# Performance work log

Hardware: AMD Instinct MI355X
Metric: run time of the kernel (lower is better)

The kernel has to match this reference:

```python
import jax, jax.numpy as jnp
import numpy as np

WS = 7      # window size
SHIFT = 3   # shift size
NH = 6      # num heads
C = 192     # channels
HH = 56
WW = 56
B = 32


def _rel_coords():
    ch, cw = np.meshgrid(np.arange(WS), np.arange(WS), indexing='ij')
    coords = np.stack([ch, cw]).reshape(2, -1)            # (2, 49)
    rel = coords[:, :, None] - coords[:, None, :]          # (2, 49, 49)
    rel[0] += WS - 1
    rel[1] += WS - 1
    rel[0] *= 2 * WS - 1
    return rel.sum(0)                                      # (49, 49)


def _swin_attn_mask(Hp, Wp):
    img = np.zeros((Hp, Wp), np.int32)
    cnt = 0
    for hs in (slice(0, -WS), slice(-WS, -SHIFT), slice(-SHIFT, None)):
        for ws_ in (slice(0, -WS), slice(-WS, -SHIFT), slice(-SHIFT, None)):
            img[hs, ws_] = cnt
            cnt += 1
    win = img.reshape(Hp // WS, WS, Wp // WS, WS).transpose(0, 2, 1, 3).reshape(-1, WS * WS)
    return win[:, :, None] != win[:, None, :]              # (Nw, 49, 49) bool


def setup_inputs() -> dict:
    key = jax.random.key(0)
    ks = jax.random.split(key, 8)
    s = 0.02
    return {
        'x': jax.random.normal(ks[0], (B, HH * WW, C), jnp.float32),
        'H': HH,
        'W': WW,
        'attn_mask': jnp.asarray(_swin_attn_mask(HH, WW)),
        'relative_coords': jnp.asarray(_rel_coords(), jnp.int32),
        'norm1_w': jnp.ones((C,), jnp.float32),
        'norm1_b': jnp.zeros((C,), jnp.float32),
        'qkv_w': jax.random.normal(ks[1], (3 * C, C), jnp.float32) * s,
        'rel_bias': jax.random.normal(ks[2], ((2 * WS - 1) ** 2, NH), jnp.float32) * 0.2,
        'proj_w': jax.random.normal(ks[3], (C, C), jnp.float32) * s,
        'proj_b': jnp.zeros((C,), jnp.float32),
        'norm2_w': jnp.ones((C,), jnp.float32),
        'norm2_b': jnp.zeros((C,), jnp.float32),
        'fc1_w': jax.random.normal(ks[4], (4 * C, C), jnp.float32) * s,
        'fc1_b': jnp.zeros((4 * C,), jnp.float32),
        'fc2_w': jax.random.normal(ks[5], (C, 4 * C), jnp.float32) * s,
        'fc2_b': jnp.zeros((C,), jnp.float32),
    }


def _ln(t, w, b):
    m = t.mean(-1, keepdims=True)
    v = t.var(-1, keepdims=True)
    return (t - m) / jnp.sqrt(v + 1e-5) * w + b


def reference(x, H, W, attn_mask, relative_coords, norm1_w, norm1_b, qkv_w, rel_bias,
              proj_w, proj_b, norm2_w, norm2_b, fc1_w, fc1_b, fc2_w, fc2_b):
    Bb, L, Cd = x.shape
    nh, hd = NH, C // NH
    shortcut = x
    h = _ln(x, norm1_w, norm1_b).reshape(Bb, H, W, Cd)
    pad_h = (WS - H % WS) % WS
    pad_w = (WS - W % WS) % WS
    if pad_h or pad_w:
        h = jnp.pad(h, ((0, 0), (0, pad_h), (0, pad_w), (0, 0)))
    Hp, Wp = H + pad_h, W + pad_w
    if SHIFT > 0:
        h = jnp.roll(h, (-SHIFT, -SHIFT), axis=(1, 2))
    nWh, nWw = Hp // WS, Wp // WS
    Lw = WS * WS
    win = h.reshape(Bb, nWh, WS, nWw, WS, Cd).transpose(0, 1, 3, 2, 4, 5).reshape(-1, Lw, Cd)
    B_ = win.shape[0]
    qkv = (win @ qkv_w.T).reshape(B_, Lw, 3, nh, hd).transpose(2, 0, 3, 1, 4)
    q, k, v = qkv[0], qkv[1], qkv[2]
    # NOTE: source multiplies by num_dim**0.5 (faithful quirk)
    attn = jnp.einsum('bhid,bhjd->bhij', q, k) * (Cd ** 0.5)
    bias = rel_bias[relative_coords].transpose(2, 0, 1)    # (nh, Lw, Lw)
    attn = attn + bias[None]
    if SHIFT > 0:
        Nw = attn_mask.shape[0]
        attn = attn.reshape(-1, Nw, nh, Lw, Lw)
        attn = jnp.where(attn_mask[None, :, None], -100.0, attn)
        attn = attn.reshape(B_, nh, Lw, Lw)
    attn = jax.nn.softmax(attn, axis=-1)
    out = jnp.einsum('bhij,bhjd->bhid', attn, v).transpose(0, 2, 1, 3).reshape(B_, Lw, Cd)
    out = out @ proj_w.T + proj_b
    out = out.reshape(Bb, nWh, nWw, WS, WS, Cd).transpose(0, 1, 3, 2, 4, 5).reshape(Bb, Hp, Wp, Cd)
    if SHIFT > 0:
        out = jnp.roll(out, (SHIFT, SHIFT), axis=(1, 2))
    out = out[:, :H, :W].reshape(Bb, L, Cd)
    x = shortcut + out
    h2 = _ln(x, norm2_w, norm2_b)
    h2 = jax.nn.gelu(h2 @ fc1_w.T + fc1_b, approximate=False)
    # source MLP applies GELU (drop2 = act_layer()) after fc2 (faithful quirk)
    h2 = jax.nn.gelu(h2 @ fc2_w.T + fc2_b, approximate=False)
    return x + h2
```

## Files before the change

### kernel.cpp

```cpp
#include <hip/hip_runtime.h>

#define WS7    7
#define SHIFT3 3
#define NHEAD  6
#define CCH    192
#define HDIM   32
#define HH56   56
#define LTOK   (HH56*HH56)
#define NWIN   64
#define NBATCH 32
#define NWTOT  (NBATCH*NWIN)
#define LW     49
#define MTOK   (NWTOT*LW)

typedef unsigned short u16;
typedef unsigned int   u32;
typedef __bf16 b16;
typedef b16   b16x8 __attribute__((ext_vector_type(8)));
typedef u16   u16x8 __attribute__((ext_vector_type(8)));
typedef float f32x4 __attribute__((ext_vector_type(4)));

__device__ __forceinline__ float b2f(u16 u) {
    u32 x = ((u32)u) << 16;
    return __builtin_bit_cast(float, x);
}
__device__ __forceinline__ u16 f2b(float f) {
    u32 x = __builtin_bit_cast(u32, f);
    u32 r = x + 0x7FFFu + ((x >> 16) & 1u);
    return (u16)(r >> 16);
}
__device__ __forceinline__ float gelu_exact(float x) {
    return 0.5f * x * (1.0f + erff(x * 0.7071067811865475f));
}

__device__ __forceinline__ int map_token(int m, int &b) {
    int widx = m / LW, p = m - widx * LW;
    b = widx >> 6;
    int wloc = widx & 63;
    int wh = wloc >> 3, ww = wloc & 7;
    int i = p / WS7, j = p - i * WS7;
    int gh = wh * WS7 + i + SHIFT3; if (gh >= HH56) gh -= HH56;
    int gw = ww * WS7 + j + SHIFT3; if (gw >= HH56) gw -= HH56;
    return gh * HH56 + gw;
}

__global__ __launch_bounds__(1024) void probe_kernel(const u16* __restrict__ x, int* flag) {
    __shared__ int ch, cz;
    if (threadIdx.x == 0) { ch = 0; cz = 0; }
    __syncthreads();
    int i = threadIdx.x * 16;
    u16x8 a = *(const u16x8*)(x + i);
    u16x8 b = *(const u16x8*)(x + i + 8);
    int h = 0, z = 0;
    #pragma unroll
    for (int q = 0; q < 8; q++) {
        h += (((a[q] >> 7) & 0xFF) >= 0xC0) + (((b[q] >> 7) & 0xFF) >= 0xC0);
        z += (a[q] == 0) + (b[q] == 0);
    }
    #pragma unroll
    for (int off = 32; off > 0; off >>= 1) {
        h += __shfl_xor(h, off, 64);
        z += __shfl_xor(z, off, 64);
    }
    if ((threadIdx.x & 63) == 0) { atomicAdd(&ch, h); atomicAdd(&cz, z); }
    __syncthreads();
    if (threadIdx.x == 0) *flag = (ch > 250 || cz > 2048) ? 1 : 0;
}

#define CANON_TOTAL 445302
__global__ __launch_bounds__(256) void canon_all_kernel(
    const int* __restrict__ flag,
    const void* s0, const void* s1, const void* s2,  const void* s3,
    const void* s4, const void* s5, const void* s6,  const void* s7,
    const void* s8, const void* s9, const void* s10, const void* s11,
    char* __restrict__ ws)
{
    int i = blockIdx.x * 256 + threadIdx.x;
    if (i >= CANON_TOTAL) return;
    const void* srcs[12] = {s0, s1, s2, s3, s4, s5, s6, s7, s8, s9, s10, s11};
    const int cnt[12] = {110592, 36864, 147456, 147456, 192, 192, 192, 192, 192, 768, 192, 1014};
    const int off[12] = {64, 221248, 294976, 589888, 884800, 885184, 885568, 885952, 886336, 886720, 888256, 888640};
    int seg = 0, base = 0;
    while (seg < 11 && i >= base + cnt[seg]) { base += cnt[seg]; seg++; }
    int j = i - base;
    const void* sp = srcs[seg];
    u16* dp = (u16*)(ws + off[seg]);
    dp[j] = (*flag) ? f2b(((const float*)sp)[j]) : ((const u16*)sp)[j];
}

__device__ __forceinline__ void stage192(const u16* __restrict__ g, int ldg, u16* s, int tid) {
    #pragma unroll
    for (int it = 0; it < 7; it++) {
        int t = it * 256 + tid;
        if (t < 1600) {
            int row = t / 25, c = t - row * 25;
            int cc = (c == 24) ? 0 : c;
            const u16* src = g + (size_t)row * ldg + cc * 8;
            u16* dst = s + (size_t)(it * 256 + (tid & ~63)) * 8;
            __builtin_amdgcn_global_load_lds(
                (const __attribute__((address_space(1))) void*)src,
                (__attribute__((address_space(3))) void*)dst, 16, 0, 0);
        }
    }
}

__device__ __forceinline__ void ln_lds_rows(u16* As, const u16* __restrict__ w,
                                            const u16* __restrict__ bia, int tid) {
    int r = tid >> 2, p = tid & 3;
    u16* row = As + r * 200 + p * 48;
    u16x8 vv[6];
    float s = 0.f, sq = 0.f;
    #pragma unroll
    for (int j = 0; j < 6; j++) {
        vv[j] = *(const u16x8*)(row + j * 8);
        #pragma unroll
        for (int q = 0; q < 8; q++) { float f = b2f(vv[j][q]); s += f; sq += f * f; }
    }
    s  += __shfl_xor(s, 1, 64);  s  += __shfl_xor(s, 2, 64);
    sq += __shfl_xor(sq, 1, 64); sq += __shfl_xor(sq, 2, 64);
    float mean = s * (1.f / 192.f);
    float var  = fmaxf(sq * (1.f / 192.f) - mean * mean, 0.f);
    float rstd = rsqrtf(var + 1e-5f);
    #pragma unroll
    for (int j = 0; j < 6; j++) {
        u16x8 o;
        #pragma unroll
        for (int q = 0; q < 8; q++) {
            int col = p * 48 + j * 8 + q;
            o[q] = f2b((b2f(vv[j][q]) - mean) * rstd * b2f(w[col]) + b2f(bia[col]));
        }
        *(u16x8*)(row + j * 8) = o;
    }
}

__device__ __forceinline__ void gather_ln(const void* __restrict__ xsrc, int isf,
                                          int mtile, const u16* __restrict__ w,
                                          const u16* __restrict__ bia,
                                          u16* As, int tid) {
    int r = tid >> 2, p = tid & 3;
    int b; int l = map_token(mtile + r, b);
    size_t rowoff = ((size_t)b * LTOK + l) * CCH + p * 48;
    float v[48];
    if (isf) {
        const float* xp = (const float*)xsrc + rowoff;
        #pragma unroll
        for (int j = 0; j < 12; j++) {
            float4 f = *(const float4*)(xp + j * 4);
            v[j * 4 + 0] = f.x; v[j * 4 + 1] = f.y;
            v[j * 4 + 2] = f.z; v[j * 4 + 3] = f.w;
        }
    } else {
        const u16* xp = (const u16*)xsrc + rowoff;
        #pragma unroll
        for (int j = 0; j < 6; j++) {
            u16x8 u = *(const u16x8*)(xp + j * 8);
            #pragma unroll
            for (int q = 0; q < 8; q++) v[j * 8 + q] = b2f(u[q]);
        }
    }
    float s = 0.f, sq = 0.f;
    #pragma unroll
    for (int j = 0; j < 48; j++) { s += v[j]; sq += v[j] * v[j]; }
    s  += __shfl_xor(s, 1, 64);  s  += __shfl_xor(s, 2, 64);
    sq += __shfl_xor(sq, 1, 64); sq += __shfl_xor(sq, 2, 64);
    float mean = s * (1.f / 192.f);
    float var  = fmaxf(sq * (1.f / 192.f) - mean * mean, 0.f);
    float rstd = rsqrtf(var + 1e-5f);
    u16* row = As + r * 200 + p * 48;
    #pragma unroll
    for (int j = 0; j < 6; j++) {
        u16x8 o;
        #pragma unroll
        for (int q = 0; q < 8; q++) {
            int col = p * 48 + j * 8 + q;
            o[q] = f2b((v[j * 8 + q] - mean) * rstd * b2f(w[col]) + b2f(bia[col]));
        }
        *(u16x8*)(row + j * 8) = o;
    }
}

template<int MODE, int NT, int LNF>
__global__ __launch_bounds__(256) void gemm_k192(
    const u16* __restrict__ A, const u16* __restrict__ Bm, int N,
    const u16* __restrict__ lnw, const u16* __restrict__ lnb,
    const u16* __restrict__ bias,
    u16* __restrict__ Cb, u16* __restrict__ X1, const void* __restrict__ Xin,
    int m_base, const int* __restrict__ flag)
{
    __shared__ __align__(16) u16 As[64 * 200];
    __shared__ __align__(16) u16 Bs[2][64 * 200];
    int isf = *flag;
    int tid = threadIdx.x;
    int m0 = blockIdx.x * 64;
    int wave = tid >> 6, lane = tid & 63;
    int wm = wave >> 1, wn = wave & 1;
    int quad = lane >> 4, mr = lane & 15;

    stage192(Bm, 192, Bs[0], tid);
    if (MODE == 0) gather_ln(Xin, isf, m_base + m0, lnw, lnb, As, tid);
    else           stage192(A + (size_t)m0 * 192, 192, As, tid);
    __syncthreads();
    if (LNF) { ln_lds_rows(As, lnw, lnb, tid); __syncthreads(); }

    const u16* pa0 = &As[(wm * 32 + mr) * 200 + quad * 8];
    #pragma unroll 1
    for (int nb = 0; nb < NT; nb++) {
        if (nb + 1 < NT)
            stage192(Bm + (size_t)(nb + 1) * 64 * 192, 192, Bs[(nb + 1) & 1], tid);
        const u16* pb0 = &Bs[nb & 1][(wn * 32 + mr) * 200 + quad * 8];
        f32x4 acc00 = {}, acc01 = {}, acc10 = {}, acc11 = {};
        #pragma unroll
        for (int ks = 0; ks < 6; ks++) {
            b16x8 a0 = __builtin_bit_cast(b16x8, *(const u16x8*)(pa0 + ks * 32));
            b16x8 a1 = __builtin_bit_cast(b16x8, *(const u16x8*)(pa0 + 16 * 200 + ks * 32));
            b16x8 b0 = __builtin_bit_cast(b16x8, *(const u16x8*)(pb0 + ks * 32));
            b16x8 b1 = __builtin_bit_cast(b16x8, *(const u16x8*)(pb0 + 16 * 200 + ks * 32));
            acc00 = __builtin_amdgcn_mfma_f32_16x16x32_bf16(a0, b0, acc00, 0, 0, 0);
            acc01 = __builtin_amdgcn_mfma_f32_16x16x32_bf16(a0, b1, acc01, 0, 0, 0);
            acc10 = __builtin_amdgcn_mfma_f32_16x16x32_bf16(a1, b0, acc10, 0, 0, 0);
            acc11 = __builtin_amdgcn_mfma_f32_16x16x32_bf16(a1, b1, acc11, 0, 0, 0);
        }
        int n0 = nb * 64;
        f32x4 accs[2][2] = {{acc00, acc01}, {acc10, acc11}};
        #pragma unroll
        for (int sm = 0; sm < 2; sm++) {
            #pragma unroll
            for (int sn = 0; sn < 2; sn++) {
                f32x4 v = accs[sm][sn];
                int nn = n0 + wn * 32 + sn * 16 + mr;
                int mb = m0 + wm * 32 + sm * 16 + quad * 4;
                #pragma unroll
                for (int r = 0; r < 4; r++) {
                    int mm = mb + r;
                    float val = v[r];
                    if (MODE == 0) {
                        Cb[(size_t)mm * N + nn] = f2b(val);
                    } else if (MODE == 1) {
                        val += b2f(bias[nn]);
                        int b; int l = map_token(m_base + mm, b);
                        size_t idx = ((size_t)b * LTOK + l) * CCH + nn;
                        float xi = isf ? ((const float*)Xin)[idx] : b2f(((const u16*)Xin)[idx]);
                        X1[idx] = f2b(xi + val);
                    } else {
                        val = gelu_exact(val + b2f(bias[nn]));
                        Cb[(size_t)mm * N + nn] = f2b(val);
                    }
                }
            }
        }
        __syncthreads();
    }
}

__global__ __launch_bounds__(256) void gemm_k768(
    const u16* __restrict__ A, const u16* __restrict__ Bm,
    const u16* __restrict__ bias, const u16* __restrict__ X1,
    void* __restrict__ Oout, size_t o_off, const int* __restrict__ flag)
{
    __shared__ __align__(16) u16 As[64 * 200];
    __shared__ __align__(16) u16 Bs[2][64 * 200];
    int isf = *flag;
    int tid = threadIdx.x;
    int m0 = blockIdx.x * 64;
    int wave = tid >> 6, lane = tid & 63;
    int wm = wave >> 1, wn = wave & 1;
    int quad = lane >> 4, mr = lane & 15;

    f32x4 acc[3][4] = {};

    const u16* pa0 = &As[(wm * 32 + mr) * 200 + quad * 8];
    #pragma unroll 1
    for (int k0 = 0; k0 < 768; k0 += 192) {
        stage192(A + (size_t)m0 * 768 + k0, 768, As, tid);
        stage192(Bm + k0, 768, Bs[0], tid);
        __syncthreads();
        #pragma unroll
        for (int nb = 0; nb < 3; nb++) {
            if (nb < 2)
                stage192(Bm + (size_t)(nb + 1) * 64 * 768 + k0, 768, Bs[(nb + 1) & 1], tid);
            const u16* pb0 = &Bs[nb & 1][(wn * 32 + mr) * 200 + quad * 8];
            #pragma unroll
            for (int ks = 0; ks < 6; ks++) {
                b16x8 a0 = __builtin_bit_cast(b16x8, *(const u16x8*)(pa0 + ks * 32));
                b16x8 a1 = __builtin_bit_cast(b16x8, *(const u16x8*)(pa0 + 16 * 200 + ks * 32));
                b16x8 b0 = __builtin_bit_cast(b16x8, *(const u16x8*)(pb0 + ks * 32));
                b16x8 b1 = __builtin_bit_cast(b16x8, *(const u16x8*)(pb0 + 16 * 200 + ks * 32));
                acc[nb][0] = __builtin_amdgcn_mfma_f32_16x16x32_bf16(a0, b0, acc[nb][0], 0, 0, 0);
                acc[nb][1] = __builtin_amdgcn_mfma_f32_16x16x32_bf16(a0, b1, acc[nb][1], 0, 0, 0);
                acc[nb][2] = __builtin_amdgcn_mfma_f32_16x16x32_bf16(a1, b0, acc[nb][2], 0, 0, 0);
                acc[nb][3] = __builtin_amdgcn_mfma_f32_16x16x32_bf16(a1, b1, acc[nb][3], 0, 0, 0);
            }
            __syncthreads();
        }
    }

    #pragma unroll
    for (int nb = 0; nb < 3; nb++) {
        #pragma unroll
        for (int sm = 0; sm < 2; sm++) {
            #pragma unroll
            for (int sn = 0; sn < 2; sn++) {
                f32x4 v = acc[nb][sm * 2 + sn];
                int nn = nb * 64 + wn * 32 + sn * 16 + mr;
                int mb = m0 + wm * 32 + sm * 16 + quad * 4;
                #pragma unroll
                for (int r = 0; r < 4; r++) {
                    int mm = mb + r;
                    float val = gelu_exact(v[r] + b2f(bias[nn]));
                    size_t idx = (size_t)mm * CCH + nn;
                    float r2 = val + b2f(X1[idx]);
                    if (isf) ((float*)Oout)[o_off + idx] = r2;
                    else     ((u16*)Oout)[o_off + idx]  = f2b(r2);
                }
            }
        }
    }
}

__global__ __launch_bounds__(256) void attn_kernel(
    const u16* __restrict__ qkv, const u16* __restrict__ rel_bias,
    u16* __restrict__ aout)
{
    __shared__ __align__(16) u16 qs[64 * 32];
    __shared__ __align__(16) u16 ks[64 * 32];
    __shared__ __align__(16) u16 vsT[32 * 72];
    __shared__ __align__(16) u16 ps[64 * 72];
    __shared__ float bias_s[169];
    int blk = blockIdx.x;
    int widx = blk / NHEAD, head = blk - widx * NHEAD;
    int wloc = widx & 63;
    int wh = wloc >> 3, ww = wloc & 7;
    int tid = threadIdx.x;
    const u16* base = qkv + (size_t)widx * LW * 576 + head * HDIM;

    if (tid < 196) {
        int i = tid >> 2, c8 = (tid & 3) * 8;
        *(uint4*)&qs[i * 32 + c8] = *(const uint4*)(base + (size_t)i * 576 + c8);
        *(uint4*)&ks[i * 32 + c8] = *(const uint4*)(base + (size_t)i * 576 + 192 + c8);
        u16x8 vv = *(const u16x8*)(base + (size_t)i * 576 + 384 + c8);
        #pragma unroll
        for (int q = 0; q < 8; q++) vsT[(c8 + q) * 72 + i] = vv[q];
    }
    for (int idx = tid; idx < 32 * 15; idx += 256) {
        int d = idx / 15, j = 49 + (idx - d * 15);
        vsT[d * 72 + j] = 0;
    }
    if (tid < 169) bias_s[tid] = b2f(rel_bias[tid * NHEAD + head]);
    __syncthreads();

    int wave = tid >> 6, lane = tid & 63;
    int quad = lane >> 4, c = lane & 15;

    b16x8 aq = __builtin_bit_cast(b16x8, *(const u16x8*)&qs[(wave * 16 + c) * 32 + quad * 8]);
    f32x4 sacc[4];
    #pragma unroll
    for (int nt = 0; nt < 4; nt++) {
        b16x8 bk = __builtin_bit_cast(b16x8, *(const u16x8*)&ks[(nt * 16 + c) * 32 + quad * 8]);
        f32x4 z = {};
        sacc[nt] = __builtin_amdgcn_mfma_f32_16x16x32_bf16(aq, bk, z, 0, 0, 0);
    }

    const float SCALE = 13.856406460551018f;
    float val[4][4];
    int rbase = wave * 16 + quad * 4;
    #pragma unroll
    for (int r = 0; r < 4; r++) {
        int i = rbase + r;
        int ih = i / WS7, iw = i - ih * WS7;
        int ri = (wh == 7 ? (ih < 4 ? 1 : 2) : 0) * 3 + (ww == 7 ? (iw < 4 ? 1 : 2) : 0);
        #pragma unroll
        for (int nt = 0; nt < 4; nt++) {
            int j = nt * 16 + c;
            float v;
            if (i >= LW) v = 0.f;
            else if (j >= LW) v = -1e30f;
            else {
                int jh = j / WS7, jw = j - jh * WS7;
                int rj = (wh == 7 ? (jh < 4 ? 1 : 2) : 0) * 3 + (ww == 7 ? (jw < 4 ? 1 : 2) : 0);
                if (ri != rj) v = -100.0f;
                else v = fmaf(sacc[nt][r], SCALE, bias_s[(ih - jh + 6) * 13 + (iw - jw + 6)]);
            }
            val[r][nt] = v;
        }
    }

    #pragma unroll
    for (int r = 0; r < 4; r++) {
        float mx = fmaxf(fmaxf(val[r][0], val[r][1]), fmaxf(val[r][2], val[r][3]));
        for (int d = 1; d < 16; d <<= 1) mx = fmaxf(mx, __shfl_xor(mx, d, 64));
        float sum = 0.f;
        #pragma unroll
        for (int nt = 0; nt < 4; nt++) { float e = expf(val[r][nt] - mx); val[r][nt] = e; sum += e; }
        for (int d = 1; d < 16; d <<= 1) sum += __shfl_xor(sum, d, 64);
        float inv = 1.f / sum;
        int i = rbase + r;
        #pragma unroll
        for (int nt = 0; nt < 4; nt++)
            ps[i * 72 + nt * 16 + c] = f2b(val[r][nt] * inv);
    }

    f32x4 oacc[2] = {{}, {}};
    #pragma unroll
    for (int kh = 0; kh < 2; kh++) {
        b16x8 ap = __builtin_bit_cast(b16x8, *(const u16x8*)&ps[(wave * 16 + c) * 72 + kh * 32 + quad * 8]);
        #pragma unroll
        for (int nt = 0; nt < 2; nt++) {
            b16x8 bv = __builtin_bit_cast(b16x8, *(const u16x8*)&vsT[(nt * 16 + c) * 72 + kh * 32 + quad * 8]);
            oacc[nt] = __builtin_amdgcn_mfma_f32_16x16x32_bf16(ap, bv, oacc[nt], 0, 0, 0);
        }
    }
    #pragma unroll
    for (int nt = 0; nt < 2; nt++) {
        #pragma unroll
        for (int r = 0; r < 4; r++) {
            int i = rbase + r;
            if (i < LW)
                aout[((size_t)widx * LW + i) * CCH + head * HDIM + nt * 16 + c] = f2b(oacc[nt][r]);
        }
    }
}

extern "C" void kernel_launch(void* const* d_in, const int* in_sizes, int n_in,
                              void* d_out, int out_size, void* d_ws, size_t ws_size,
                              hipStream_t stream)
{
    const void* x_in = d_in[0];
    char* ws = (char*)d_ws;
    int* flag = (int*)ws;

    u16* qkvw_c  = (u16*)(ws + 64);
    u16* projw_c = (u16*)(ws + 221248);
    u16* fc1w_c  = (u16*)(ws + 294976);
    u16* fc2w_c  = (u16*)(ws + 589888);
    u16* n1w_c   = (u16*)(ws + 884800);
    u16* n1b_c   = (u16*)(ws + 885184);
    u16* n2w_c   = (u16*)(ws + 885568);
    u16* n2b_c   = (u16*)(ws + 885952);
    u16* projb_c = (u16*)(ws + 886336);
    u16* fc1b_c  = (u16*)(ws + 886720);
    u16* fc2b_c  = (u16*)(ws + 888256);
    u16* relb_c  = (u16*)(ws + 888640);

    const size_t P0 = 1u << 20;
    const size_t X1SZ   = (size_t)MTOK * CCH * 2;
    const size_t QKVSZ  = (size_t)MTOK * 576 * 2;
    const size_t H1FULL = (size_t)MTOK * 768 * 2;

    u16* x1 = (u16*)(ws + P0);

    probe_kernel<<<1, 1024, 0, stream>>>((const u16*)x_in, flag);
    canon_all_kernel<<<(CANON_TOTAL + 255) / 256, 256, 0, stream>>>(
        flag,
        d_in[7], d_in[9], d_in[13], d_in[15],
        d_in[5], d_in[6], d_in[11], d_in[12],
        d_in[10], d_in[14], d_in[16], d_in[8],
        ws);

    int QC, EC;
    u16 *aoutb, *qkvq, *h1q;
    if (ws_size >= P0 + 2 * X1SZ + H1FULL) {
        QC = 1; EC = 1;
        aoutb = (u16*)(ws + P0 + X1SZ);
        qkvq  = (u16*)(ws + P0 + 2 * X1SZ);
        h1q   = qkvq;
    } else if (ws_size >= P0 + 2 * X1SZ + QKVSZ) {
        QC = 1; EC = 2;
        aoutb = (u16*)(ws + P0 + X1SZ);
        qkvq  = (u16*)(ws + P0 + 2 * X1SZ);
        h1q   = qkvq;
    } else {
        QC = 4; EC = 8;
        aoutb = (u16*)(ws + P0 + X1SZ);
        qkvq  = (u16*)(ws + P0 + X1SZ + 9633792);
        h1q   = (u16*)(ws + P0 + X1SZ);
    }

    const int MQ = MTOK / QC;
    const int ME = MTOK / EC;

    for (int q = 0; q < QC; q++) {
        int mb = q * MQ;
        gemm_k192<0, 9, 0><<<MQ / 64, 256, 0, stream>>>(
            nullptr, qkvw_c, 576, n1w_c, n1b_c, nullptr, qkvq, nullptr, x_in, mb, flag);
        attn_kernel<<<(NWTOT / QC) * NHEAD, 256, 0, stream>>>(qkvq, relb_c, aoutb);
        gemm_k192<1, 3, 0><<<MQ / 64, 256, 0, stream>>>(
            aoutb, projw_c, 192, nullptr, nullptr, projb_c, nullptr, x1, x_in, mb, flag);
    }

    for (int e = 0; e < EC; e++) {
        size_t off = (size_t)e * ME * CCH;
        gemm_k192<2, 12, 1><<<ME / 64, 256, 0, stream>>>(
            x1 + off, fc1w_c, 768, n2w_c, n2b_c, fc1b_c, h1q, nullptr, nullptr, 0, flag);
        gemm_k768<<<ME / 64, 256, 0, stream>>>(
            h1q, fc2w_c, fc2b_c, x1 + off, d_out, off, flag);
    }
}
```

Measured before the change: 581.2 us.

## Rewrite fc2 GEMM with 128x192 tiles and async LDS double buffering

Replaces the fc2 GEMM (K=768) with a new templated kernel that uses 128x192 output tiles, a K-step of 32 and double-buffered shared memory. Tiles are filled with direct global-to-LDS loads using an XOR swizzle to avoid bank conflicts. The aim is more MFMA work per LDS read and overlap of the next tile's loads with the current step's math, replacing the old kernel that re-staged B three times per 192-wide K chunk. The trade-offs are higher register pressure from 24 accumulators per thread and half as many blocks, and correctness depends on the hand-written vmcnt waits.

```diff
diff --git a/kernel.cpp b/kernel.cpp
--- a/kernel.cpp
+++ b/kernel.cpp
@@ -252,66 +252,95 @@
     }
 }
 
-__global__ __launch_bounds__(256) void gemm_k768(
+template<int ROWS>
+__device__ __forceinline__ void stageL(const u16* __restrict__ g, int ldk, u16* s, int tid) {
+    constexpr int ITER = ROWS * 4 / 256;
+    #pragma unroll
+    for (int it = 0; it < ITER; it++) {
+        int t = it * 256 + tid;
+        int row = t >> 2, c = t & 3;
+        int cc = c ^ ((row >> 1) & 3);
+        const u16* src = g + (size_t)row * ldk + cc * 8;
+        u16* dst = s + (size_t)(it * 256 + (tid & ~63)) * 8;
+        __builtin_amdgcn_global_load_lds(
+            (const __attribute__((address_space(1))) void*)src,
+            (__attribute__((address_space(3))) void*)dst, 16, 0, 0);
+    }
+}
+
+template<int KK>
+__global__ __launch_bounds__(256, 3) void gemm_t3(
     const u16* __restrict__ A, const u16* __restrict__ Bm,
-    const u16* __restrict__ bias, const u16* __restrict__ X1,
-    void* __restrict__ Oout, size_t o_off, const int* __restrict__ flag)
+    const u16* __restrict__ bias,
+    const u16* __restrict__ X1,
+    void* __restrict__ Oout, size_t o_off,
+    const int* __restrict__ flag)
 {
-    __shared__ __align__(16) u16 As[64 * 200];
-    __shared__ __align__(16) u16 Bs[2][64 * 200];
-    int isf = *flag;
+    __shared__ __align__(16) u16 As[2][128 * 32];
+    __shared__ __align__(16) u16 Bs[2][192 * 32];
     int tid = threadIdx.x;
-    int m0 = blockIdx.x * 64;
+    int m0 = blockIdx.x * 128, n0 = blockIdx.y * 192;
     int wave = tid >> 6, lane = tid & 63;
     int wm = wave >> 1, wn = wave & 1;
     int quad = lane >> 4, mr = lane & 15;
 
-    f32x4 acc[3][4] = {};
-
-    const u16* pa0 = &As[(wm * 32 + mr) * 200 + quad * 8];
+    const u16* Ag = A + (size_t)m0 * KK;
+    const u16* Bg = Bm + (size_t)n0 * KK;
+
+    stageL<128>(Ag, KK, As[0], tid);
+    stageL<192>(Bg, KK, Bs[0], tid);
+
+    f32x4 acc[4][6] = {};
+    constexpr int NSTEP = KK / 32;
+
     #pragma unroll 1
-    for (int k0 = 0; k0 < 768; k0 += 192) {
-        stage192(A + (size_t)m0 * 768 + k0, 768, As, tid);
-        stage192(Bm + k0, 768, Bs[0], tid);
-        __syncthreads();
-        #pragma unroll
-        for (int nb = 0; nb < 3; nb++) {
-            if (nb < 2)
-                stage192(Bm + (size_t)(nb + 1) * 64 * 768 + k0, 768, Bs[(nb + 1) & 1], tid);
-            const u16* pb0 = &Bs[nb & 1][(wn * 32 + mr) * 200 + quad * 8];
+    for (int t = 0; t < NSTEP; t++) {
+        int cur = t & 1;
+        if (t + 1 < NSTEP) {
+            stageL<128>(Ag + (t + 1) * 32, KK, As[cur ^ 1], tid);
+            stageL<192>(Bg + (t + 1) * 32, KK, Bs[cur ^ 1], tid);
+            asm volatile("s_waitcnt vmcnt(5)");
+        } else {
+            asm volatile("s_waitcnt vmcnt(0)");
+        }
+        __builtin_amdgcn_s_barrier();
+        __builtin_amdgcn_sched_barrier(0);
+        b16x8 a[4], b[6];
+        #pragma unroll
+        for (int sm = 0; sm < 4; sm++) {
+            int row = wm * 64 + sm * 16 + mr;
+            a[sm] = __builtin_bit_cast(b16x8,
+                *(const u16x8*)&As[cur][row * 32 + (quad ^ ((row >> 1) & 3)) * 8]);
+        }
+        #pragma unroll
+        for (int sn = 0; sn < 6; sn++) {
+            int row = wn * 96 + sn * 16 + mr;
+            b[sn] = __builtin_bit_cast(b16x8,
+                *(const u16x8*)&Bs[cur][row * 32 + (quad ^ ((row >> 1) & 3)) * 8]);
+        }
+        #pragma unroll
+        for (int sm = 0; sm < 4; sm++)
             #pragma unroll
-            for (int ks = 0; ks < 6; ks++) {
-                b16x8 a0 = __builtin_bit_cast(b16x8, *(const u16x8*)(pa0 + ks * 32));
-                b16x8 a1 = __builtin_bit_cast(b16x8, *(const u16x8*)(pa0 + 16 * 200 + ks * 32));
-                b16x8 b0 = __builtin_bit_cast(b16x8, *(const u16x8*)(pb0 + ks * 32));
-                b16x8 b1 = __builtin_bit_cast(b16x8, *(const u16x8*)(pb0 + 16 * 200 + ks * 32));
-                acc[nb][0] = __builtin_amdgcn_mfma_f32_16x16x32_bf16(a0, b0, acc[nb][0], 0, 0, 0);
-                acc[nb][1] = __builtin_amdgcn_mfma_f32_16x16x32_bf16(a0, b1, acc[nb][1], 0, 0, 0);
-                acc[nb][2] = __builtin_amdgcn_mfma_f32_16x16x32_bf16(a1, b0, acc[nb][2], 0, 0, 0);
-                acc[nb][3] = __builtin_amdgcn_mfma_f32_16x16x32_bf16(a1, b1, acc[nb][3], 0, 0, 0);
-            }
-            __syncthreads();
-        }
-    }
-
-    #pragma unroll
-    for (int nb = 0; nb < 3; nb++) {
-        #pragma unroll
-        for (int sm = 0; sm < 2; sm++) {
+            for (int sn = 0; sn < 6; sn++)
+                acc[sm][sn] = __builtin_amdgcn_mfma_f32_16x16x32_bf16(a[sm], b[sn], acc[sm][sn], 0, 0, 0);
+        __builtin_amdgcn_sched_barrier(0);
+        __builtin_amdgcn_s_barrier();
+    }
+
+    int isf = *flag;
+    #pragma unroll
+    for (int sm = 0; sm < 4; sm++) {
+        #pragma unroll
+        for (int r = 0; r < 4; r++) {
+            int mm = m0 + wm * 64 + sm * 16 + quad * 4 + r;
             #pragma unroll
-            for (int sn = 0; sn < 2; sn++) {
-                f32x4 v = acc[nb][sm * 2 + sn];
-                int nn = nb * 64 + wn * 32 + sn * 16 + mr;
-                int mb = m0 + wm * 32 + sm * 16 + quad * 4;
-                #pragma unroll
-                for (int r = 0; r < 4; r++) {
-                    int mm = mb + r;
-                    float val = gelu_exact(v[r] + b2f(bias[nn]));
-                    size_t idx = (size_t)mm * CCH + nn;
-                    float r2 = val + b2f(X1[idx]);
-                    if (isf) ((float*)Oout)[o_off + idx] = r2;
-                    else     ((u16*)Oout)[o_off + idx]  = f2b(r2);
-                }
+            for (int sn = 0; sn < 6; sn++) {
+                int nn = n0 + wn * 96 + sn * 16 + mr;
+                float val = gelu_exact(acc[sm][sn][r] + b2f(bias[nn]));
+                size_t idx = (size_t)mm * CCH + nn;
+                float r2 = val + b2f(X1[idx]);
+                if (isf) ((float*)Oout)[o_off + idx] = r2;
+                else     ((u16*)Oout)[o_off + idx]  = f2b(r2);
             }
         }
     }
@@ -491,7 +520,7 @@
         size_t off = (size_t)e * ME * CCH;
         gemm_k192<2, 12, 1><<<ME / 64, 256, 0, stream>>>(
             x1 + off, fc1w_c, 768, n2w_c, n2b_c, fc1b_c, h1q, nullptr, nullptr, 0, flag);
-        gemm_k768<<<ME / 64, 256, 0, stream>>>(
+        gemm_t3<768><<<dim3(ME / 128, 1), 256, 0, stream>>>(
             h1q, fc2w_c, fc2b_c, x1 + off, d_out, off, flag);
     }
 }
```

New measurement: 587.7 us. About the same (+1.1%).
